# Performance work log

Hardware: AMD Instinct MI355X
Metric: run time of the kernel (lower is better)

## Reference

```python
import jax, jax.numpy as jnp
import numpy as np

B, NP, C_IN, H = 8, 6250, 512, 256   # graphs, nodes/graph, in-feat, hidden
EPG = 100000                          # edges per graph
K = 5000                              # ceil(0.8 * NP) kept by TopKPooling
H3 = 3 * H


def setup_inputs() -> dict:
    key = jax.random.key(0)
    ks = jax.random.split(key, 16)
    N, E = B * NP, B * EPG
    x = jax.random.normal(ks[0], (N, C_IN), jnp.float32)
    offs = (jnp.arange(E) // EPG) * NP  # keep edges inside their graph
    src = jax.random.randint(ks[1], (E,), 0, NP) + offs
    dst = jax.random.randint(ks[2], (E,), 0, NP) + offs
    edge_index = jnp.stack([src, dst]).astype(jnp.int64)
    edge_attr = jax.random.uniform(ks[3], (E,), jnp.float32)
    batch = jnp.repeat(jnp.arange(B), NP).astype(jnp.int64)
    s = 0.05
    W1 = jax.random.normal(ks[4], (C_IN, H), jnp.float32) * s
    b1 = jnp.zeros((H,), jnp.float32)
    W2 = jax.random.normal(ks[5], (H, H), jnp.float32) * s
    b2 = jnp.zeros((H,), jnp.float32)
    pw = jax.random.normal(ks[6], (H3,), jnp.float32) * s   # TopKPooling attn vector
    lw1 = jax.random.normal(ks[7], (H3 * 2, H), jnp.float32) * s
    lb1 = jnp.zeros((H,), jnp.float32)
    lw2 = jax.random.normal(ks[8], (H, H // 2), jnp.float32) * s
    lb2 = jnp.zeros((H // 2,), jnp.float32)
    lw3 = jax.random.normal(ks[9], (H // 2, 3), jnp.float32) * s
    lb3 = jnp.zeros((3,), jnp.float32)
    return {"x": x, "edge_index": edge_index, "edge_attr": edge_attr, "batch": batch,
            "W1": W1, "b1": b1, "W2": W2, "b2": b2, "pw": pw,
            "lw1": lw1, "lb1": lb1, "lw2": lw2, "lb2": lb2, "lw3": lw3, "lb3": lb3}


def _gcn(x, W, b, src, dst, ew, n):
    xw = x @ W
    deg = jnp.zeros((n,), xw.dtype).at[dst].add(ew) + 1.0
    dinv = jax.lax.rsqrt(deg)
    norm = dinv[src] * ew * dinv[dst]
    out = jnp.zeros_like(xw).at[dst].add(norm[:, None] * xw[src])
    return out + (dinv * dinv)[:, None] * xw + b


def reference(x, edge_index, edge_attr, batch, W1, b1, W2, b2, pw,
              lw1, lb1, lw2, lb2, lw3, lb3):
    N = x.shape[0]
    src, dst = edge_index[0], edge_index[1]
    x1 = jax.nn.relu(_gcn(x, W1, b1, src, dst, edge_attr, N))
    x2 = jax.nn.relu(_gcn(x1, W2, b2, src, dst, edge_attr, N))
    x3 = jax.nn.relu(_gcn(x2, W2, b2, src, dst, edge_attr, N))  # conv2 reused (as in source)
    cat_x = jnp.concatenate([x1, x2, x3], axis=1)               # [N, 3H]
    # TopKPooling: score = sigmoid((x . w) / ||w||), keep top-K per graph, scale by score
    score = jax.nn.sigmoid((cat_x @ pw) / jnp.linalg.norm(pw))   # [N]
    sc = score.reshape(B, NP)
    topv, topi = jax.lax.top_k(sc, K)                            # [B, K]
    xg = cat_x.reshape(B, NP, H3)
    sel = jnp.take_along_axis(xg, topi[:, :, None], axis=1) * topv[:, :, None]  # [B, K, 3H]
    readout = jnp.concatenate([sel.mean(axis=1), sel.max(axis=1)], axis=1)      # [B, 6H]
    h = jax.nn.relu(readout @ lw1 + lb1)
    h = jax.nn.relu(h @ lw2 + lb2)       # dropout p=0 is a no-op
    return h @ lw3 + lb3                 # [B, 3]
```

## Files before the change

kernel.cpp:

```cpp
#include <hip/hip_runtime.h>
#include <stdint.h>

#define NODES  50000
#define MPAD   50048
#define NGRAPH 8
#define NP_G   6250
#define EPG    100000
#define EDGES  800000
#define KKEEP  5000
#define HID    256
#define CIN    512
#define H3     768
#define SCANB  196
#define RCHUNK 200
#define MLPCH  24
#define MLPCK  64
#define ESL    3125

#define K1_HIST  512
#define K1_CAST  25000
#define K1_W1    512
#define K1_W2    256
#define K1_TOTAL (K1_HIST + K1_CAST + K1_W1 + K1_W2 + 1)
#define GEMM_GRID 1568
#define FILL_GRID 256

using f32x4  = __attribute__((ext_vector_type(4))) float;
using bf16x8 = __attribute__((ext_vector_type(8))) short;
using u16x8  = __attribute__((ext_vector_type(8))) unsigned short;
typedef unsigned short u16;
typedef unsigned int   u32;
typedef unsigned long long u64;

__device__ __forceinline__ float bf2f(u16 u) {
    return __uint_as_float(((uint32_t)u) << 16);
}
__device__ __forceinline__ u16 f2bf(float f) {
    uint32_t u = __float_as_uint(f);
    u += 0x7fffu + ((u >> 16) & 1u);
    return (u16)(u >> 16);
}

__global__ __launch_bounds__(256) void k1_kernel(
        const int* __restrict__ ei, const float* __restrict__ ew,
        u64* __restrict__ partial,
        const float* __restrict__ x, u16* __restrict__ A0,
        const float* __restrict__ W1, const float* __restrict__ W2,
        const float* __restrict__ pw,
        u16* __restrict__ Wt1, u16* __restrict__ Wt2, float* __restrict__ invn) {
    __shared__ __align__(16) char smem[ESL * 8];
    int b = blockIdx.x, t = threadIdx.x;
    if (b < K1_HIST) {
        u64* hl = (u64*)smem;
        int g  = b >> 6;
        int r  = b & 63;
        int bb = r >> 1;
        int h  = r & 1;
        for (int k = t; k < ESL; k += 256) hl[k] = 0ull;
        __syncthreads();
        int ebase = g * EPG + bb * ESL;
        int lo = h * ESL;
        for (int k = t; k < ESL; k += 256) {
            int e = ebase + k;
            int d = ei[EDGES + e];
            int il = d - g * NP_G - lo;
            if ((unsigned)il < (unsigned)ESL) {
                u64 enc = (1ull << 48) | (u64)(ew[e] * 4294967296.0f);
                atomicAdd(&hl[il], enc);
            }
        }
        __syncthreads();
        u64* prow = partial + (size_t)(g * 32 + bb) * NP_G + lo;
        for (int k = t; k < ESL; k += 256) prow[k] = hl[k];
    } else if (b < K1_HIST + K1_CAST) {
        size_t base = ((size_t)(b - K1_HIST) * 256 + t) * 4;
        float4 v = *(const float4*)(x + base);
        ushort4 o;
        o.x = f2bf(v.x); o.y = f2bf(v.y); o.z = f2bf(v.z); o.w = f2bf(v.w);
        *(ushort4*)(A0 + base) = o;
    } else if (b < K1_HIST + K1_CAST + K1_W1) {
        int id = (b - K1_HIST - K1_CAST) * 256 + t;
        int n = id >> 9, k = id & 511;
        Wt1[id] = f2bf(W1[(size_t)k * HID + n]);
    } else if (b < K1_TOTAL - 1) {
        int id = (b - K1_HIST - K1_CAST - K1_W1) * 256 + t;
        int n = id >> 8, k = id & 255;
        Wt2[id] = f2bf(W2[(size_t)k * HID + n]);
    } else {
        float* sh = (float*)smem;
        float s = 0.f;
        for (int i = t; i < H3; i += 256) { float v = pw[i]; s += v * v; }
        sh[t] = s; __syncthreads();
        for (int off = 128; off; off >>= 1) {
            if (t < off) sh[t] += sh[t + off];
            __syncthreads();
        }
        if (t == 0) invn[0] = rsqrtf(sh[0]);
    }
}

__global__ void scan1_kernel(const u64* __restrict__ partial,
                             u32* __restrict__ blockbase,
                             int* __restrict__ iscan, int* __restrict__ bsum,
                             float* __restrict__ dinv) {
    int b = blockIdx.x, t = threadIdx.x;
    int i = b * 256 + t;
    int c = 0;
    if (i < NODES) {
        int g = i / NP_G, il = i - g * NP_G;
        size_t base = (size_t)(g * 32) * NP_G + il;
        u64 fix = 0ull; u32 cnt = 0;
#pragma unroll 4
        for (int j = 0; j < 32; ++j) {
            size_t idx = base + (size_t)j * NP_G;
            u64 pv = partial[idx];
            blockbase[idx] = cnt;
            cnt += (u32)(pv >> 48);
            fix += pv & 0xFFFFFFFFFFFFull;
        }
        c = (int)cnt;
        float deg = (float)fix * (1.0f / 4294967296.0f);
        dinv[i] = rsqrtf(deg + 1.0f);
    }
    int lane = t & 63, wv = t >> 6;
    int v = c;
    for (int off = 1; off < 64; off <<= 1) {
        int u = __shfl_up(v, off);
        if (lane >= off) v += u;
    }
    __shared__ int ws[4];
    if (lane == 63) ws[wv] = v;
    __syncthreads();
    if (t == 0) { int s = 0; for (int k = 0; k < 4; k++) { int tmp = ws[k]; ws[k] = s; s += tmp; } }
    __syncthreads();
    v += ws[wv];
    if (i < NODES) iscan[i] = v - c;
    if (t == 255) bsum[b] = v;
}

__global__ void scan3_kernel(const int* __restrict__ iscan, const int* __restrict__ bsum,
                             int* __restrict__ rowptr) {
    int b = blockIdx.x, t = threadIdx.x;
    int v = (t < b) ? bsum[t] : 0;
    for (int off = 1; off < 64; off <<= 1) v += __shfl_xor(v, off, 64);
    __shared__ int ws[4];
    if ((t & 63) == 0) ws[t >> 6] = v;
    __syncthreads();
    int boffb = ws[0] + ws[1] + ws[2] + ws[3];
    int i = b * 256 + t;
    if (i > NODES) return;
    if (i == NODES) { rowptr[NODES] = EDGES; return; }
    rowptr[i] = boffb + iscan[i];
}

__device__ __forceinline__ bool gemm_map64(int i, int& bm, int& bn) {
    int g = i & 7, s = i >> 3;
    int b0 = (6250 * g + 63) >> 6;
    int b1 = (6250 * (g + 1) + 63) >> 6;
    int t = b0 + (s >> 1);
    if (t >= b1) return false;
    bm = t;
    bn = s & 1;
    return true;
}

__device__ __forceinline__ void gemm64_body(const u16* __restrict__ A,
                                            const u16* __restrict__ Bt,
                                            u16* __restrict__ C,
                                            int K, int bm, int bn,
                                            u16* As, u16* Bs) {
    const int tid  = threadIdx.x;
    const int wave = tid >> 6, lane = tid & 63;
    const int quad = lane >> 4, l16 = lane & 15;
    const int sr = tid >> 2;
    const int sc = tid & 3;
    const int swz = (sc ^ ((sr >> 1) & 3)) * 8;
    const int rphys = (quad ^ ((l16 >> 1) & 3)) * 8;

    const u16* Ag = A + (size_t)(bm * 64 + sr) * K + sc * 8;
    const u16* Bg = Bt + (size_t)(bn * 128 + sr) * K + sc * 8;

    f32x4 acc[4][2];
#pragma unroll
    for (int i = 0; i < 4; i++)
#pragma unroll
        for (int j = 0; j < 2; j++) { f32x4 z = {0.f, 0.f, 0.f, 0.f}; acc[i][j] = z; }

    for (int k0 = 0; k0 < K; k0 += 32) {
        int4 av0 = *(const int4*)(Ag + k0);
        int4 bv0 = *(const int4*)(Bg + k0);
        int4 bv1 = *(const int4*)(Bg + (size_t)64 * K + k0);
        __syncthreads();
        *(int4*)(As + sr * 32 + swz)        = av0;
        *(int4*)(Bs + sr * 32 + swz)        = bv0;
        *(int4*)(Bs + (sr + 64) * 32 + swz) = bv1;
        __syncthreads();
        bf16x8 af[4], bfr[2];
#pragma unroll
        for (int i = 0; i < 4; i++)
            af[i] = *(const bf16x8*)(As + (i * 16 + l16) * 32 + rphys);
#pragma unroll
        for (int j = 0; j < 2; j++)
            bfr[j] = *(const bf16x8*)(Bs + (wave * 32 + j * 16 + l16) * 32 + rphys);
#pragma unroll
        for (int i = 0; i < 4; i++)
#pragma unroll
            for (int j = 0; j < 2; j++)
                acc[i][j] = __builtin_amdgcn_mfma_f32_16x16x32_bf16(af[i], bfr[j], acc[i][j], 0, 0, 0);
    }

    const int crow0 = bm * 64 + quad * 4;
    const int ccol0 = bn * 128 + wave * 32 + l16;
#pragma unroll
    for (int i = 0; i < 4; i++)
#pragma unroll
        for (int j = 0; j < 2; j++)
#pragma unroll
            for (int r = 0; r < 4; r++)
                C[(size_t)(crow0 + i * 16 + r) * HID + ccol0 + j * 16] = f2bf(acc[i][j][r]);
}

__global__ __launch_bounds__(256) void k2_kernel(
        const u16* __restrict__ A0, const u16* __restrict__ Wt1,
        u16* __restrict__ C) {
    __shared__ u16 As[64 * 32];
    __shared__ u16 Bs[128 * 32];
    int bm, bn;
    if (!gemm_map64(blockIdx.x, bm, bn)) return;
    gemm64_body(A0, Wt1, C, CIN, bm, bn, As, Bs);
}

__global__ __launch_bounds__(256) void gemm_bt(const u16* __restrict__ A,
                                               const u16* __restrict__ Bt,
                                               u16* __restrict__ C, int K) {
    __shared__ u16 As[64 * 32];
    __shared__ u16 Bs[128 * 32];
    int bm, bn;
    if (!gemm_map64(blockIdx.x, bm, bn)) return;
    gemm64_body(A, Bt, C, K, bm, bn, As, Bs);
}

__global__ __launch_bounds__(256) void fill_kernel(
        const int* __restrict__ ei, const float* __restrict__ ew,
        const float* __restrict__ dinv, const int* __restrict__ rowptr,
        const u32* __restrict__ blockbase, int2* __restrict__ csr) {
    __shared__ u32 cursor[ESL];
    int g  = blockIdx.x & 7;
    int bb = blockIdx.x >> 3;
    const u32* bbase = blockbase + (size_t)(g * 32 + bb) * NP_G;
    const int* rp = rowptr + g * NP_G;
    int ebase = g * EPG + bb * ESL;
    for (int h = 0; h < 2; ++h) {
        int lo = h * ESL;
        for (int k = threadIdx.x; k < ESL; k += 256)
            cursor[k] = (u32)rp[lo + k] + bbase[lo + k];
        __syncthreads();
#pragma unroll 4
        for (int k = threadIdx.x; k < ESL; k += 256) {
            int e = ebase + k;
            int d = ei[EDGES + e];
            int il = d - g * NP_G - lo;
            if ((unsigned)il < (unsigned)ESL) {
                int s = ei[e];
                u32 pos = atomicAdd(&cursor[il], 1u);
                csr[pos] = make_int2(s, __float_as_int(dinv[s] * ew[e] * dinv[d]));
            }
        }
        __syncthreads();
    }
}

template<bool SCORE>
__global__ void agg_kernel(const u16* __restrict__ xw, u16* __restrict__ xo,
                           const int* __restrict__ rowptr, const int2* __restrict__ csr,
                           const float* __restrict__ dinv, const float* __restrict__ bias,
                           const u16* __restrict__ xs1, const u16* __restrict__ xs2,
                           const float* __restrict__ pw, const float* __restrict__ invn,
                           float* __restrict__ score, u64* __restrict__ keys) {
    int wave = threadIdx.x >> 6;
    int lane = threadIdx.x & 63;
    int g  = blockIdx.x & 7;
    int nl = (blockIdx.x >> 3) * 4 + wave;
    if (nl >= NP_G) return;
    int w = g * NP_G + nl;
    int half = lane >> 5;
    int f8 = (lane & 31) * 8;
    size_t ro = (size_t)w * HID + f8;

    float acc0[8], acc1[8];
#pragma unroll
    for (int j = 0; j < 8; ++j) { acc0[j] = 0.f; acc1[j] = 0.f; }

    int p = rowptr[w], p1 = rowptr[w + 1];
    for (int q = p; q < p1; q += 64) {
        int m = min(64, p1 - q);
        int2 e = make_int2(0, 0);
        if (lane < m) e = csr[q + lane];
        int j = 0;
        for (; j + 8 <= m; j += 8) {
            int i0 = j + half,     i1 = j + 2 + half;
            int i2 = j + 4 + half, i3 = j + 6 + half;
            int   s0 = __shfl(e.x, i0, 64); float w0 = __int_as_float(__shfl(e.y, i0, 64));
            int   s1 = __shfl(e.x, i1, 64); float w1 = __int_as_float(__shfl(e.y, i1, 64));
            int   s2 = __shfl(e.x, i2, 64); float w2 = __int_as_float(__shfl(e.y, i2, 64));
            int   s3 = __shfl(e.x, i3, 64); float w3 = __int_as_float(__shfl(e.y, i3, 64));
            u16x8 v0 = *(const u16x8*)(xw + (size_t)s0 * HID + f8);
            u16x8 v1 = *(const u16x8*)(xw + (size_t)s1 * HID + f8);
            u16x8 v2 = *(const u16x8*)(xw + (size_t)s2 * HID + f8);
            u16x8 v3 = *(const u16x8*)(xw + (size_t)s3 * HID + f8);
#pragma unroll
            for (int t = 0; t < 8; ++t) {
                acc0[t] += w0 * bf2f(v0[t]);
                acc1[t] += w1 * bf2f(v1[t]);
                acc0[t] += w2 * bf2f(v2[t]);
                acc1[t] += w3 * bf2f(v3[t]);
            }
        }
        for (; j + 2 <= m; j += 2) {
            int i0 = j + half;
            int s0 = __shfl(e.x, i0, 64); float w0 = __int_as_float(__shfl(e.y, i0, 64));
            u16x8 v0 = *(const u16x8*)(xw + (size_t)s0 * HID + f8);
#pragma unroll
            for (int t = 0; t < 8; ++t) acc0[t] += w0 * bf2f(v0[t]);
        }
        if (j < m) {
            int s0 = __shfl(e.x, j, 64); float w0 = __int_as_float(__shfl(e.y, j, 64));
            w0 = half ? 0.f : w0;
            u16x8 v0 = *(const u16x8*)(xw + (size_t)s0 * HID + f8);
#pragma unroll
            for (int t = 0; t < 8; ++t) acc0[t] += w0 * bf2f(v0[t]);
        }
    }

#pragma unroll
    for (int j = 0; j < 8; ++j) {
        acc0[j] += acc1[j];
        acc0[j] += __shfl(acc0[j], lane ^ 32, 64);
    }

    float di = dinv[w], sw = di * di;
    u16x8 sv = *(const u16x8*)(xw + ro);
    float bb[8];
    {
        float4 t0 = *(const float4*)(bias + f8);
        float4 t1 = *(const float4*)(bias + f8 + 4);
        bb[0] = t0.x; bb[1] = t0.y; bb[2] = t0.z; bb[3] = t0.w;
        bb[4] = t1.x; bb[5] = t1.y; bb[6] = t1.z; bb[7] = t1.w;
    }
    u16x8 o;
    float ov[8];
#pragma unroll
    for (int j = 0; j < 8; ++j) {
        float v = fmaxf(acc0[j] + sw * bf2f(sv[j]) + bb[j], 0.f);
        o[j] = f2bf(v);
        ov[j] = bf2f(o[j]);
    }
    if (half == 0) *(u16x8*)(xo + ro) = o;

    if (SCORE) {
        u16x8 v1 = *(const u16x8*)(xs1 + ro);
        u16x8 v2 = *(const u16x8*)(xs2 + ro);
        float acc = 0.f;
#pragma unroll
        for (int j = 0; j < 8; ++j) {
            acc += bf2f(v1[j]) * pw[f8 + j];
            acc += bf2f(v2[j]) * pw[256 + f8 + j];
            acc += ov[j]       * pw[512 + f8 + j];
        }
#pragma unroll
        for (int off = 1; off < 32; off <<= 1) acc += __shfl_xor(acc, off, 64);
        if (lane == 0) {
            float s = acc * invn[0];
            float sc = 1.f / (1.f + __expf(-s));
            score[w] = sc;
            keys[w] = ((u64)__float_as_uint(sc) << 13) | (unsigned int)(NP_G - 1 - nl);
        }
    }
}

__global__ __launch_bounds__(1024) void selcomp_kernel(
        const u64* __restrict__ keys, const float* __restrict__ score,
        int* __restrict__ selidx, float* __restrict__ selscr) {
    __shared__ u64 kk[NP_G];
    __shared__ unsigned int hist[4][256];
    __shared__ unsigned int sfx[257];
    __shared__ u64 spref;
    __shared__ unsigned int swant;
    int g = blockIdx.x, t = threadIdx.x;
    const u64* kg = keys + (size_t)g * NP_G;
    for (int i = t; i < NP_G; i += 1024) kk[i] = kg[i];
    if (t == 0) { spref = 0ull; swant = KKEEP; }
    const int wgrp = (t >> 8) & 3;
    u64 mask = 0ull;
    __syncthreads();
    for (int shift = 40; shift >= 0; shift -= 8) {
        if (t < 256) { hist[0][t] = 0; hist[1][t] = 0; hist[2][t] = 0; hist[3][t] = 0; }
        __syncthreads();
        u64 pref = spref;
        for (int i = t; i < NP_G; i += 1024) {
            u64 key = kk[i];
            if ((key & mask) == pref)
                atomicAdd(&hist[wgrp][(unsigned int)(key >> shift) & 255u], 1u);
        }
        __syncthreads();
        if (t < 256) sfx[t] = hist[0][t] + hist[1][t] + hist[2][t] + hist[3][t];
        if (t == 0) sfx[256] = 0;
        __syncthreads();
        for (int off = 1; off < 256; off <<= 1) {
            unsigned int v = 0;
            if (t < 256 && t + off < 256) v = sfx[t + off];
            __syncthreads();
            if (t < 256 && t + off < 256) sfx[t] += v;
            __syncthreads();
        }
        unsigned int want = swant;
        __syncthreads();
        if (t < 256) {
            unsigned int s0 = sfx[t], s1 = sfx[t + 1];
            if (s0 >= want && s1 < want) {
                spref = pref | ((u64)t << shift);
                swant = want - s1;
            }
        }
        __syncthreads();
        mask |= (255ull << shift);
    }
    u64 kth = spref;
    int lane = t & 63, wv = t >> 6;
    __shared__ int wsum[16];
    __shared__ int cbase;
    if (t == 0) cbase = 0;
    __syncthreads();
    for (int k = 0; k < (NP_G + 1023) / 1024; ++k) {
        int i = k * 1024 + t;
        bool sel = (i < NP_G) && (kk[i] >= kth);
        int n = g * NP_G + i;
        u64 bal = __ballot(sel);
        int prefix = __popcll(bal & ((1ull << lane) - 1ull));
        if (lane == 0) wsum[wv] = __popcll(bal);
        __syncthreads();
        if (t == 0) {
            int s = cbase;
            for (int j = 0; j < 16; ++j) { int tmp = wsum[j]; wsum[j] = s; s += tmp; }
            cbase = s;
        }
        __syncthreads();
        if (sel) {
            int pos = wsum[wv] + prefix;
            selidx[g * KKEEP + pos] = n;
            selscr[g * KKEEP + pos] = score[n];
        }
        __syncthreads();
    }
}

__global__ __launch_bounds__(256) void readout_kernel(
        const u16* __restrict__ x1, const u16* __restrict__ x2,
        const u16* __restrict__ x3,
        const int* __restrict__ selidx, const float* __restrict__ selscr,
        float* __restrict__ sumbuf, int* __restrict__ maxbuf) {
    int g = blockIdx.x, tpart = blockIdx.y, c = blockIdx.z;
    int fcol = threadIdx.x;
    const u16* xt = (tpart == 0) ? x1 : ((tpart == 1) ? x2 : x3);
    __shared__ int   sidx[RCHUNK];
    __shared__ float sscr[RCHUNK];
    int base = g * KKEEP + c * RCHUNK;
    if (fcol < RCHUNK) { sidx[fcol] = selidx[base + fcol]; sscr[fcol] = selscr[base + fcol]; }
    __syncthreads();
    float sum = 0.f, mx = 0.f;
#pragma unroll 1
    for (int j = 0; j < RCHUNK; j += 4) {
        int n0 = sidx[j], n1 = sidx[j + 1], n2 = sidx[j + 2], n3 = sidx[j + 3];
        float s0 = sscr[j], s1 = sscr[j + 1], s2 = sscr[j + 2], s3 = sscr[j + 3];
        float v0 = bf2f(xt[(size_t)n0 * HID + fcol]) * s0;
        float v1 = bf2f(xt[(size_t)n1 * HID + fcol]) * s1;
        float v2 = bf2f(xt[(size_t)n2 * HID + fcol]) * s2;
        float v3 = bf2f(xt[(size_t)n3 * HID + fcol]) * s3;
        sum += v0 + v1 + v2 + v3;
        mx = fmaxf(mx, fmaxf(fmaxf(v0, v1), fmaxf(v2, v3)));
    }
    int o = (g * 3 + tpart) * HID + fcol;
    atomicAdd(&sumbuf[o], sum);
    atomicMax(&maxbuf[o], __float_as_int(mx));
}

__global__ __launch_bounds__(256) void mlp1_kernel(const float* __restrict__ sumbuf,
                                                   const int* __restrict__ maxbuf,
                                                   const float* __restrict__ lw1,
                                                   float* __restrict__ h1acc) {
    int g = blockIdx.x, ch = blockIdx.y, t = threadIdx.x;
    __shared__ float r[MLPCK];
    int k0 = ch * MLPCK;
    if (t < MLPCK) {
        int i = k0 + t;
        r[t] = (i < 768) ? sumbuf[g * 768 + i] * (1.f / 5000.f)
                         : __int_as_float(maxbuf[g * 768 + (i - 768)]);
    }
    __syncthreads();
    float a0 = 0.f, a1 = 0.f, a2 = 0.f, a3 = 0.f;
#pragma unroll
    for (int i = 0; i < MLPCK; i += 4) {
        a0 += r[i]     * lw1[(size_t)(k0 + i)     * 256 + t];
        a1 += r[i + 1] * lw1[(size_t)(k0 + i + 1) * 256 + t];
        a2 += r[i + 2] * lw1[(size_t)(k0 + i + 2) * 256 + t];
        a3 += r[i + 3] * lw1[(size_t)(k0 + i + 3) * 256 + t];
    }
    atomicAdd(&h1acc[g * 256 + t], (a0 + a1) + (a2 + a3));
}

__global__ __launch_bounds__(256) void mlp2_kernel(const float* __restrict__ h1acc,
                                                   const float* __restrict__ lb1,
                                                   const float* __restrict__ lw2,
                                                   const float* __restrict__ lb2,
                                                   const float* __restrict__ lw3,
                                                   const float* __restrict__ lb3,
                                                   float* __restrict__ out) {
    __shared__ float h1[256];
    __shared__ float part[256];
    __shared__ float h2[128];
    int g = blockIdx.x, t = threadIdx.x;
    h1[t] = fmaxf(h1acc[g * 256 + t] + lb1[t], 0.f);
    __syncthreads();
    int col = t & 127, half = t >> 7;
    float a = 0.f;
#pragma unroll
    for (int i = 0; i < 128; i += 4) {
        int k = half * 128 + i;
        a += h1[k]     * lw2[k * 128 + col]
           + h1[k + 1] * lw2[(k + 1) * 128 + col]
           + h1[k + 2] * lw2[(k + 2) * 128 + col]
           + h1[k + 3] * lw2[(k + 3) * 128 + col];
    }
    part[t] = a;
    __syncthreads();
    if (t < 128) h2[t] = fmaxf(part[t] + part[t + 128] + lb2[t], 0.f);
    __syncthreads();
    if (t < 3) {
        float a3 = lb3[t];
        for (int i = 0; i < 128; ++i) a3 += h2[i] * lw3[i * 3 + t];
        out[g * 3 + t] = a3;
    }
}

extern "C" void kernel_launch(void* const* d_in, const int* in_sizes, int n_in,
                              void* d_out, int out_size, void* d_ws, size_t ws_size,
                              hipStream_t stream) {
    const float* x   = (const float*)d_in[0];
    const int*   ei  = (const int*)d_in[1];
    const float* ew  = (const float*)d_in[2];
    const float* W1  = (const float*)d_in[4];
    const float* b1  = (const float*)d_in[5];
    const float* W2  = (const float*)d_in[6];
    const float* b2  = (const float*)d_in[7];
    const float* pw  = (const float*)d_in[8];
    const float* lw1 = (const float*)d_in[9];
    const float* lb1 = (const float*)d_in[10];
    const float* lw2 = (const float*)d_in[11];
    const float* lb2 = (const float*)d_in[12];
    const float* lw3 = (const float*)d_in[13];
    const float* lb3 = (const float*)d_in[14];
    float* out = (float*)d_out;

    char* p = (char*)d_ws;
    auto alloc = [&](size_t bytes) -> char* {
        char* r = p;
        p += (bytes + 255) & ~(size_t)255;
        return r;
    };
    u16* A0  = (u16*)alloc((size_t)MPAD * CIN * 2);
    u16* x3  = (u16*)alloc((size_t)MPAD * HID * 2);
    u16* xw  = (u16*)alloc((size_t)MPAD * HID * 2);
    u16* Wt1 = (u16*)alloc((size_t)HID * CIN * 2);
    u16* Wt2 = (u16*)alloc((size_t)HID * HID * 2);
    int2*  csr    = (int2*)alloc((size_t)EDGES * 8);
    u64*   partial   = (u64*)alloc((size_t)256 * NP_G * 8);
    u32*   blockbase = (u32*)alloc((size_t)256 * NP_G * 4);
    int*   rowptr = (int*)alloc((size_t)(NODES + 1) * 4);
    int*   iscan  = (int*)alloc((size_t)NODES * 4);
    int*   bsum   = (int*)alloc((size_t)SCANB * 4);
    u64*   keys   = (u64*)alloc((size_t)NODES * 8);
    float* score  = (float*)alloc((size_t)NODES * 4);
    float* dinv   = (float*)alloc((size_t)NODES * 4);
    int*   selidx = (int*)alloc((size_t)NGRAPH * KKEEP * 4);
    float* selscr = (float*)alloc((size_t)NGRAPH * KKEEP * 4);
    float* invn   = (float*)alloc(256);
    char* zbase = p;
    float* sumbuf = (float*)alloc(6144 * 4);
    int*   maxbuf = (int*)alloc(6144 * 4);
    float* h1acc  = (float*)alloc((size_t)NGRAPH * 256 * 4);
    size_t zbytes = (size_t)(p - zbase);

    u16* x1 = A0;
    u16* x2 = A0 + (size_t)MPAD * HID;

    hipMemsetAsync(zbase, 0, zbytes, stream);

    k1_kernel<<<K1_TOTAL, 256, 0, stream>>>(ei, ew, partial, x, A0,
                                            W1, W2, pw, Wt1, Wt2, invn);
    scan1_kernel<<<SCANB, 256, 0, stream>>>(partial, blockbase, iscan, bsum, dinv);
    scan3_kernel<<<SCANB + 1, 256, 0, stream>>>(iscan, bsum, rowptr);
    k2_kernel<<<GEMM_GRID, 256, 0, stream>>>(A0, Wt1, xw);
    fill_kernel<<<FILL_GRID, 256, 0, stream>>>(ei, ew, dinv, rowptr, blockbase, csr);

    int aggBlocks = 8 * ((NP_G + 3) / 4);

    agg_kernel<false><<<aggBlocks, 256, 0, stream>>>(xw, x1, rowptr, csr, dinv, b1,
                                                     nullptr, nullptr, nullptr, nullptr,
                                                     nullptr, nullptr);
    gemm_bt<<<GEMM_GRID, 256, 0, stream>>>(x1, Wt2, xw, HID);
    agg_kernel<false><<<aggBlocks, 256, 0, stream>>>(xw, x2, rowptr, csr, dinv, b2,
                                                     nullptr, nullptr, nullptr, nullptr,
                                                     nullptr, nullptr);
    gemm_bt<<<GEMM_GRID, 256, 0, stream>>>(x2, Wt2, xw, HID);
    agg_kernel<true><<<aggBlocks, 256, 0, stream>>>(xw, x3, rowptr, csr, dinv, b2,
                                                    x1, x2, pw, invn, score, keys);

    selcomp_kernel<<<NGRAPH, 1024, 0, stream>>>(keys, score, selidx, selscr);
    readout_kernel<<<dim3(NGRAPH, 3, KKEEP / RCHUNK), 256, 0, stream>>>(
        x1, x2, x3, selidx, selscr, sumbuf, maxbuf);
    mlp1_kernel<<<dim3(NGRAPH, MLPCH), 256, 0, stream>>>(sumbuf, maxbuf, lw1, h1acc);
    mlp2_kernel<<<NGRAPH, 256, 0, stream>>>(h1acc, lb1, lw2, lb2, lw3, lb3, out);
}
```

Before: 469.0 us.

## Merge CSR fill into layer-1 GEMM launch, prefetch GEMM tiles, simplify agg tail

```diff
diff --git a/kernel.cpp b/kernel.cpp
--- a/kernel.cpp
+++ b/kernel.cpp
@@ -24,6 +24,7 @@
 #define K1_TOTAL (K1_HIST + K1_CAST + K1_W1 + K1_W2 + 1)
 #define GEMM_GRID 1568
 #define FILL_GRID 256
+#define K2_TOTAL  (GEMM_GRID + FILL_GRID)
 
 using f32x4  = __attribute__((ext_vector_type(4))) float;
 using bf16x8 = __attribute__((ext_vector_type(8))) short;
@@ -186,15 +187,21 @@
 #pragma unroll
         for (int j = 0; j < 2; j++) { f32x4 z = {0.f, 0.f, 0.f, 0.f}; acc[i][j] = z; }
 
+    int4 av  = *(const int4*)(Ag);
+    int4 bv0 = *(const int4*)(Bg);
+    int4 bv1 = *(const int4*)(Bg + (size_t)64 * K);
+
     for (int k0 = 0; k0 < K; k0 += 32) {
-        int4 av0 = *(const int4*)(Ag + k0);
-        int4 bv0 = *(const int4*)(Bg + k0);
-        int4 bv1 = *(const int4*)(Bg + (size_t)64 * K + k0);
-        __syncthreads();
-        *(int4*)(As + sr * 32 + swz)        = av0;
+        __syncthreads();
+        *(int4*)(As + sr * 32 + swz)        = av;
         *(int4*)(Bs + sr * 32 + swz)        = bv0;
         *(int4*)(Bs + (sr + 64) * 32 + swz) = bv1;
         __syncthreads();
+        if (k0 + 32 < K) {
+            av  = *(const int4*)(Ag + k0 + 32);
+            bv0 = *(const int4*)(Bg + k0 + 32);
+            bv1 = *(const int4*)(Bg + (size_t)64 * K + k0 + 32);
+        }
         bf16x8 af[4], bfr[2];
 #pragma unroll
         for (int i = 0; i < 4; i++)
@@ -221,13 +228,44 @@
 }
 
 __global__ __launch_bounds__(256) void k2_kernel(
-        const u16* __restrict__ A0, const u16* __restrict__ Wt1,
-        u16* __restrict__ C) {
-    __shared__ u16 As[64 * 32];
-    __shared__ u16 Bs[128 * 32];
-    int bm, bn;
-    if (!gemm_map64(blockIdx.x, bm, bn)) return;
-    gemm64_body(A0, Wt1, C, CIN, bm, bn, As, Bs);
+        const u16* __restrict__ A0, const u16* __restrict__ Wt1, u16* __restrict__ xw,
+        const int* __restrict__ ei, const float* __restrict__ ew,
+        const float* __restrict__ dinv, const int* __restrict__ rowptr,
+        const u32* __restrict__ blockbase, int2* __restrict__ csr) {
+    __shared__ __align__(16) char smem[12544];
+    int b = blockIdx.x;
+    if (b < GEMM_GRID) {
+        int bm, bn;
+        if (!gemm_map64(b, bm, bn)) return;
+        u16* As = (u16*)smem;
+        u16* Bs = (u16*)(smem + 4096);
+        gemm64_body(A0, Wt1, xw, CIN, bm, bn, As, Bs);
+    } else {
+        u32* cursor = (u32*)smem;
+        int g  = b & 7;
+        int bb = (b - GEMM_GRID) >> 3;
+        const u32* bbase = blockbase + (size_t)(g * 32 + bb) * NP_G;
+        const int* rp = rowptr + g * NP_G;
+        int ebase = g * EPG + bb * ESL;
+        for (int h = 0; h < 2; ++h) {
+            int lo = h * ESL;
+            for (int k = threadIdx.x; k < ESL; k += 256)
+                cursor[k] = (u32)rp[lo + k] + bbase[lo + k];
+            __syncthreads();
+#pragma unroll 4
+            for (int k = threadIdx.x; k < ESL; k += 256) {
+                int e = ebase + k;
+                int d = ei[EDGES + e];
+                int il = d - g * NP_G - lo;
+                if ((unsigned)il < (unsigned)ESL) {
+                    int s = ei[e];
+                    u32 pos = atomicAdd(&cursor[il], 1u);
+                    csr[pos] = make_int2(s, __float_as_int(dinv[s] * ew[e] * dinv[d]));
+                }
+            }
+            __syncthreads();
+        }
+    }
 }
 
 __global__ __launch_bounds__(256) void gemm_bt(const u16* __restrict__ A,
@@ -238,36 +276,6 @@
     int bm, bn;
     if (!gemm_map64(blockIdx.x, bm, bn)) return;
     gemm64_body(A, Bt, C, K, bm, bn, As, Bs);
-}
-
-__global__ __launch_bounds__(256) void fill_kernel(
-        const int* __restrict__ ei, const float* __restrict__ ew,
-        const float* __restrict__ dinv, const int* __restrict__ rowptr,
-        const u32* __restrict__ blockbase, int2* __restrict__ csr) {
-    __shared__ u32 cursor[ESL];
-    int g  = blockIdx.x & 7;
-    int bb = blockIdx.x >> 3;
-    const u32* bbase = blockbase + (size_t)(g * 32 + bb) * NP_G;
-    const int* rp = rowptr + g * NP_G;
-    int ebase = g * EPG + bb * ESL;
-    for (int h = 0; h < 2; ++h) {
-        int lo = h * ESL;
-        for (int k = threadIdx.x; k < ESL; k += 256)
-            cursor[k] = (u32)rp[lo + k] + bbase[lo + k];
-        __syncthreads();
-#pragma unroll 4
-        for (int k = threadIdx.x; k < ESL; k += 256) {
-            int e = ebase + k;
-            int d = ei[EDGES + e];
-            int il = d - g * NP_G - lo;
-            if ((unsigned)il < (unsigned)ESL) {
-                int s = ei[e];
-                u32 pos = atomicAdd(&cursor[il], 1u);
-                csr[pos] = make_int2(s, __float_as_int(dinv[s] * ew[e] * dinv[d]));
-            }
-        }
-        __syncthreads();
-    }
 }
 
 template<bool SCORE>
@@ -296,14 +304,19 @@
         int m = min(64, p1 - q);
         int2 e = make_int2(0, 0);
         if (lane < m) e = csr[q + lane];
-        int j = 0;
-        for (; j + 8 <= m; j += 8) {
+        for (int j = 0; j < m; j += 8) {
             int i0 = j + half,     i1 = j + 2 + half;
             int i2 = j + 4 + half, i3 = j + 6 + half;
-            int   s0 = __shfl(e.x, i0, 64); float w0 = __int_as_float(__shfl(e.y, i0, 64));
-            int   s1 = __shfl(e.x, i1, 64); float w1 = __int_as_float(__shfl(e.y, i1, 64));
-            int   s2 = __shfl(e.x, i2, 64); float w2 = __int_as_float(__shfl(e.y, i2, 64));
-            int   s3 = __shfl(e.x, i3, 64); float w3 = __int_as_float(__shfl(e.y, i3, 64));
+            int c0 = min(i0, m - 1), c1 = min(i1, m - 1);
+            int c2 = min(i2, m - 1), c3 = min(i3, m - 1);
+            int   s0 = __shfl(e.x, c0, 64);
+            int   s1 = __shfl(e.x, c1, 64);
+            int   s2 = __shfl(e.x, c2, 64);
+            int   s3 = __shfl(e.x, c3, 64);
+            float w0 = (i0 < m) ? __int_as_float(__shfl(e.y, c0, 64)) : 0.f;
+            float w1 = (i1 < m) ? __int_as_float(__shfl(e.y, c1, 64)) : 0.f;
+            float w2 = (i2 < m) ? __int_as_float(__shfl(e.y, c2, 64)) : 0.f;
+            float w3 = (i3 < m) ? __int_as_float(__shfl(e.y, c3, 64)) : 0.f;
             u16x8 v0 = *(const u16x8*)(xw + (size_t)s0 * HID + f8);
             u16x8 v1 = *(const u16x8*)(xw + (size_t)s1 * HID + f8);
             u16x8 v2 = *(const u16x8*)(xw + (size_t)s2 * HID + f8);
@@ -315,20 +328,6 @@
                 acc0[t] += w2 * bf2f(v2[t]);
                 acc1[t] += w3 * bf2f(v3[t]);
             }
-        }
-        for (; j + 2 <= m; j += 2) {
-            int i0 = j + half;
-            int s0 = __shfl(e.x, i0, 64); float w0 = __int_as_float(__shfl(e.y, i0, 64));
-            u16x8 v0 = *(const u16x8*)(xw + (size_t)s0 * HID + f8);
-#pragma unroll
-            for (int t = 0; t < 8; ++t) acc0[t] += w0 * bf2f(v0[t]);
-        }
-        if (j < m) {
-            int s0 = __shfl(e.x, j, 64); float w0 = __int_as_float(__shfl(e.y, j, 64));
-            w0 = half ? 0.f : w0;
-            u16x8 v0 = *(const u16x8*)(xw + (size_t)s0 * HID + f8);
-#pragma unroll
-            for (int t = 0; t < 8; ++t) acc0[t] += w0 * bf2f(v0[t]);
         }
     }
 
@@ -599,8 +598,8 @@
                                             W1, W2, pw, Wt1, Wt2, invn);
     scan1_kernel<<<SCANB, 256, 0, stream>>>(partial, blockbase, iscan, bsum, dinv);
     scan3_kernel<<<SCANB + 1, 256, 0, stream>>>(iscan, bsum, rowptr);
-    k2_kernel<<<GEMM_GRID, 256, 0, stream>>>(A0, Wt1, xw);
-    fill_kernel<<<FILL_GRID, 256, 0, stream>>>(ei, ew, dinv, rowptr, blockbase, csr);
+    k2_kernel<<<K2_TOTAL, 256, 0, stream>>>(A0, Wt1, xw, ei, ew, dinv, rowptr,
+                                            blockbase, csr);
 
     int aggBlocks = 8 * ((NP_G + 3) / 4);
 
```

After: 452.6 us. 1.04x faster.
